# Kernel optimization log

Hardware: AMD Instinct MI355X
Metric: run time of the kernel (lower is better)

## Reference

```python
import jax, jax.numpy as jnp
import numpy as np
import math

B, SEQ, PRED, F, DM, NH, DFF, S, DMARK = 16, 336, 96, 7, 512, 8, 2048, 16, 5
EL, DL = 2, 1
DH = DM // NH


def _pe(max_len, d):
    pos = np.arange(max_len)[:, None].astype(np.float32)
    div = np.exp(np.arange(0, d, 2).astype(np.float32) * (-math.log(10000.0) / d))
    pe = np.zeros((max_len, d), np.float32)
    pe[:, 0::2] = np.sin(pos * div)
    pe[:, 1::2] = np.cos(pos * div)
    return jnp.asarray(pe)


def _make_tao():
    t = np.ones((S, S), np.float32)
    t[:, 0] = 0.0
    t[:, -1] = 0.0
    t[1] *= -1.0
    t[0] = 0.0
    t[0, 0] = 1.0
    t[2:, 1:-1] = np.eye(S - 2, dtype=np.float32)
    return jnp.asarray(t)


PE = _pe(2000, DM)
TAO = _make_tao()
ZVEC = jnp.zeros((S,), jnp.float32).at[:2].set(1.0)
MASK = jnp.triu(jnp.full((PRED, PRED), -1e9, jnp.float32), k=1)  # causal additive mask


def _ln(x, w, b, eps=1e-5):
    m = x.mean(-1, keepdims=True)
    v = ((x - m) ** 2).mean(-1, keepdims=True)
    return (x - m) * jax.lax.rsqrt(v + eps) * w + b


def _mha(q_in, kv_in, qkv_w, qkv_b, ow, ob, mask=None):
    wq, wk, wv = jnp.split(qkv_w, 3, axis=0)
    bq, bk, bv = jnp.split(qkv_b, 3, axis=0)

    def proj(x, w, bb):
        y = x @ w.T + bb  # [B, T, DM]
        return y.reshape(y.shape[0], y.shape[1], NH, DH).transpose(0, 2, 1, 3)

    q, k, v = proj(q_in, wq, bq), proj(kv_in, wk, bk), proj(kv_in, wv, bv)
    s = jnp.einsum('bhqd,bhkd->bhqk', q, k) / math.sqrt(DH)
    if mask is not None:
        s = s + mask
    a = jax.nn.softmax(s, axis=-1)
    o = jnp.einsum('bhqk,bhkd->bhqd', a, v)
    o = o.transpose(0, 2, 1, 3).reshape(q_in.shape)
    return o @ ow.T + ob


def _per_feature(xe, xd, eqw, eqb, eow, eob, el1w, el1b, el2w, el2b,
                 ef1w, ef1b, ef2w, ef2b, elw, elb,
                 dsqw, dsqb, dsow, dsob, dcqw, dcqb, dcow, dcob,
                 dl1w, dl1b, dl2w, dl2b, dl3w, dl3b, df1w, df1b, df2w, df2b):
    # post-norm TransformerEncoder (relu FFN), eval mode (no dropout)
    h = xe
    for l in range(EL):
        h = _ln(h + _mha(h, h, eqw[l], eqb[l], eow[l], eob[l]), el1w[l], el1b[l])
        ff = jax.nn.relu(h @ ef1w[l].T + ef1b[l]) @ ef2w[l].T + ef2b[l]
        h = _ln(h + ff, el2w[l], el2b[l])
    # encoder_linear maps time axis seqlen -> prelen
    mem = jnp.einsum('bsd,ps->bpd', h, elw) + elb[None, :, None]
    t = xd
    for l in range(DL):
        t = _ln(t + _mha(t, t, dsqw[l], dsqb[l], dsow[l], dsob[l], MASK), dl1w[l], dl1b[l])
        t = _ln(t + _mha(t, mem, dcqw[l], dcqb[l], dcow[l], dcob[l]), dl2w[l], dl2b[l])
        ff = jax.nn.relu(t @ df1w[l].T + df1b[l]) @ df2w[l].T + df2b[l]
        t = _ln(t + ff, dl3w[l], dl3b[l])
    return t


_vfeat = jax.vmap(_per_feature, in_axes=(1, 1) + (0,) * 32, out_axes=1)


def setup_inputs():
    key = jax.random.key(0)
    ks = iter(jax.random.split(key, 64))

    def rn(shape, s=0.05):
        return jax.random.normal(next(ks), shape, jnp.float32) * s

    return {
        'batch_x': rn((B, SEQ, F), 1.0),
        'batch_x_mark': rn((B, SEQ, DMARK - 1), 1.0),
        'batch_y': rn((B, PRED, F), 1.0),
        'batch_y_mark': rn((B, PRED, DMARK - 1), 1.0),
        'w_in': rn((DM, DMARK)), 'b_in': rn((DM,)),
        'w_co': rn((DM, DMARK - 1)), 'b_co': rn((DM,)),
        'eqw': rn((F, EL, 3 * DM, DM)), 'eqb': rn((F, EL, 3 * DM)),
        'eow': rn((F, EL, DM, DM)), 'eob': rn((F, EL, DM)),
        'el1w': jnp.ones((F, EL, DM)), 'el1b': jnp.zeros((F, EL, DM)),
        'el2w': jnp.ones((F, EL, DM)), 'el2b': jnp.zeros((F, EL, DM)),
        'ef1w': rn((F, EL, DFF, DM)), 'ef1b': rn((F, EL, DFF)),
        'ef2w': rn((F, EL, DM, DFF)), 'ef2b': rn((F, EL, DM)),
        'elw': rn((F, PRED, SEQ)), 'elb': rn((F, PRED)),
        'dsqw': rn((F, DL, 3 * DM, DM)), 'dsqb': rn((F, DL, 3 * DM)),
        'dsow': rn((F, DL, DM, DM)), 'dsob': rn((F, DL, DM)),
        'dcqw': rn((F, DL, 3 * DM, DM)), 'dcqb': rn((F, DL, 3 * DM)),
        'dcow': rn((F, DL, DM, DM)), 'dcob': rn((F, DL, DM)),
        'dl1w': jnp.ones((F, DL, DM)), 'dl1b': jnp.zeros((F, DL, DM)),
        'dl2w': jnp.ones((F, DL, DM)), 'dl2b': jnp.zeros((F, DL, DM)),
        'dl3w': jnp.ones((F, DL, DM)), 'dl3b': jnp.zeros((F, DL, DM)),
        'df1w': rn((F, DL, DFF, DM)), 'df1b': rn((F, DL, DFF)),
        'df2w': rn((F, DL, DM, DFF)), 'df2b': rn((F, DL, DM)),
        'wc': rn((S, DM)), 'bc': rn((S,)),
        'ws': rn((1, DM)), 'bs': rn((1,)),
    }


def reference(batch_x, batch_x_mark, batch_y, batch_y_mark,
              w_in, b_in, w_co, b_co,
              eqw, eqb, eow, eob, el1w, el1b, el2w, el2b,
              ef1w, ef1b, ef2w, ef2b, elw, elb,
              dsqw, dsqb, dsow, dsob, dcqw, dcqb, dcow, dcob,
              dl1w, dl1b, dl2w, dl2b, dl3w, dl3b, df1w, df1b, df2w, df2b,
              wc, bc, ws, bs):
    Bsz = batch_x.shape[0]
    # time marks are shared across features -> broadcast instead of concat loop
    hist = jnp.concatenate(
        [batch_x[..., None],
         jnp.broadcast_to(batch_x_mark[:, :, None, :], (Bsz, SEQ, F, DMARK - 1))], axis=-1)
    fut = jnp.broadcast_to(batch_y_mark[:, -PRED:, None, :], (Bsz, PRED, F, DMARK - 1))
    hist = hist.transpose(0, 2, 1, 3)  # [B, F, SEQ, DMARK]
    fut = fut.transpose(0, 2, 1, 3)    # [B, F, PRED, DMARK-1]
    xe = hist @ w_in.T + b_in + PE[:SEQ]
    xd = fut @ w_co.T + b_co + PE[:PRED]
    dec = _vfeat(xe, xd, eqw, eqb, eow, eob, el1w, el1b, el2w, el2b,
                 ef1w, ef1b, ef2w, ef2b, elw, elb,
                 dsqw, dsqb, dsow, dsob, dcqw, dcqb, dcow, dcob,
                 dl1w, dl1b, dl2w, dl2b, dl3w, dl3b, df1w, df1b, df2w, df2b)
    # g_c = Linear + Hardsigmoid; g_s = Linear + Softplus
    c = jnp.clip((jnp.einsum('bfpd,sd->bfps', dec, wc) + bc) / 6.0 + 0.5, 0.0, 1.0)
    sig = jax.nn.softplus(jnp.einsum('bfpd,d->bfp', dec, ws[0]) + bs[0])
    # linear state recurrence a = TAO @ a + c, y = z^T a, scanned over prediction days
    a0 = c[:, :, 0]                      # [B, F, S] (torch initializes a with day-0 g_c)
    cs = jnp.moveaxis(c, 2, 0)           # [PRED, B, F, S]
    ss = jnp.moveaxis(sig, 2, 0)         # [PRED, B, F]

    def step(a, xs):
        cd, sd = xs
        a = jnp.einsum('ij,bfj->bfi', TAO, a) + cd
        return a, jnp.einsum('s,bfs->bf', ZVEC, a) + sd

    _, ys = jax.lax.scan(step, a0, (cs, ss))
    return jnp.transpose(ys, (1, 0, 2))  # [B, PRED, F]
```

## Files before the change

kernel.cpp:

```cpp
#include <hip/hip_runtime.h>

typedef unsigned short u16;
typedef unsigned int   u32;
typedef __attribute__((ext_vector_type(8))) short short8;
typedef __attribute__((ext_vector_type(4))) float f32x4;

#define DEV static __device__ __forceinline__

DEV float bf2f(u16 u) { return __uint_as_float(((u32)u) << 16); }
DEV u16 f2bf(float f) {
  u32 u = __float_as_uint(f);
  return (u16)((u + 0x7fffu + ((u >> 16) & 1u)) >> 16);
}

#define GLD16(gp, lp) __builtin_amdgcn_global_load_lds( \
    (__attribute__((address_space(1))) u32*)(gp),       \
    (__attribute__((address_space(3))) u32*)(lp), 16, 0, 0)

__global__ __launch_bounds__(256) void gemm_bf16(
    const u16* __restrict__ A, const u16* __restrict__ Bw, u16* __restrict__ C,
    const float* __restrict__ bias, int M, int N, int K,
    long sAz, long sBz, long sCz, long sBiasZ, int relu)
{
  __shared__ __align__(16) u16 Asm[128 * 32];
  __shared__ __align__(16) u16 Bsm[128 * 32];
  int z = blockIdx.z;
  A += (size_t)z * sAz; Bw += (size_t)z * sBz; C += (size_t)z * sCz; bias += (size_t)z * sBiasZ;
  int tileM = blockIdx.x * 128, tileN = blockIdx.y * 128;
  int tid = threadIdx.x, wave = tid >> 6, lane = tid & 63;

  const u16* gA = A + (size_t)(tileM + wave * 16 + (lane >> 2)) * K + (lane & 3) * 8;
  const u16* gB = Bw + (size_t)(tileN + wave * 16 + (lane >> 2)) * K + (lane & 3) * 8;
  u16* lA = Asm + wave * 512 + lane * 8;
  u16* lB = Bsm + wave * 512 + lane * 8;

  f32x4 acc[4][4] = {};

  int wm = (wave & 1) * 64, wn = (wave >> 1) * 64;
  int lr = lane & 15, lk = (lane >> 4) * 8;
  const u16* ra = Asm + (wm + lr) * 32 + lk;
  const u16* rb = Bsm + (wn + lr) * 32 + lk;

  for (int kt = 0; kt < K; kt += 32) {
    GLD16(gA, lA); GLD16(gA + (size_t)64 * K, lA + 2048);
    GLD16(gB, lB); GLD16(gB + (size_t)64 * K, lB + 2048);
    gA += 32; gB += 32;
    __syncthreads();
    short8 av[4], bv[4];
    #pragma unroll
    for (int i = 0; i < 4; i++) av[i] = *(const short8*)(ra + i * 512);
    #pragma unroll
    for (int j = 0; j < 4; j++) bv[j] = *(const short8*)(rb + j * 512);
    #pragma unroll
    for (int i = 0; i < 4; i++)
      #pragma unroll
      for (int j = 0; j < 4; j++)
        acc[i][j] = __builtin_amdgcn_mfma_f32_16x16x32_bf16(av[i], bv[j], acc[i][j], 0, 0, 0);
    __syncthreads();
  }

  #pragma unroll
  for (int j = 0; j < 4; j++) {
    int ncol = tileN + wn + j * 16 + lr;
    float bb = bias[ncol];
    #pragma unroll
    for (int i = 0; i < 4; i++) {
      int mrow = tileM + wm + i * 16 + (lane >> 4) * 4;
      #pragma unroll
      for (int r = 0; r < 4; r++) {
        float v = acc[i][j][r] + bb;
        if (relu) v = fmaxf(v, 0.f);
        C[(size_t)(mrow + r) * N + ncol] = f2bf(v);
      }
    }
  }
}

__global__ void cvt_w_kernel(const float* __restrict__ src, u16* __restrict__ dst,
                             long n_per_f, long f_stride, long total4)
{
  long i = (long)blockIdx.x * blockDim.x + threadIdx.x;
  long step = (long)gridDim.x * blockDim.x;
  for (; i < total4; i += step) {
    long e = i * 4;
    long f = e / n_per_f; long r = e - f * n_per_f;
    float4 v = *(const float4*)(src + f * f_stride + r);
    *(ushort4*)(dst + e) = make_ushort4(f2bf(v.x), f2bf(v.y), f2bf(v.z), f2bf(v.w));
  }
}

__global__ __launch_bounds__(128) void embed_enc_k(
    const float* __restrict__ x, const float* __restrict__ mark,
    const float* __restrict__ w_in, const float* __restrict__ b_in,
    u16* __restrict__ hb)
{
  int row = blockIdx.x;
  int f = row / 5376; int rem = row - f * 5376; int b = rem / 336; int s = rem - b * 336;
  int bsix = b * 336 + s;
  float v0 = x[(size_t)bsix * 7 + f];
  float m0 = mark[(size_t)bsix * 4 + 0], m1 = mark[(size_t)bsix * 4 + 1];
  float m2 = mark[(size_t)bsix * 4 + 2], m3 = mark[(size_t)bsix * 4 + 3];
  int d0 = threadIdx.x * 4;
  u16 ob[4];
  #pragma unroll
  for (int c = 0; c < 4; c++) {
    int d = d0 + c;
    const float* w = w_in + d * 5;
    float val = w[0] * v0 + w[1] * m0 + w[2] * m1 + w[3] * m2 + w[4] * m3 + b_in[d];
    int i = d >> 1;
    float dv = expf((float)i * -0.0359778920778f);
    float arg = (float)s * dv;
    val += (d & 1) ? cosf(arg) : sinf(arg);
    ob[c] = f2bf(val);
  }
  *(ushort4*)(hb + (size_t)row * 512 + d0) = make_ushort4(ob[0], ob[1], ob[2], ob[3]);
}

__global__ __launch_bounds__(128) void embed_dec_k(
    const float* __restrict__ ymark, const float* __restrict__ w_co,
    const float* __restrict__ b_co, u16* __restrict__ tb)
{
  int row = blockIdx.x;
  int f = row / 1536; int rem = row - f * 1536; int b = rem / 96; int pp = rem - b * 96;
  int bp = b * 96 + pp;
  float m0 = ymark[(size_t)bp * 4 + 0], m1 = ymark[(size_t)bp * 4 + 1];
  float m2 = ymark[(size_t)bp * 4 + 2], m3 = ymark[(size_t)bp * 4 + 3];
  int d0 = threadIdx.x * 4;
  u16 ob[4];
  #pragma unroll
  for (int c = 0; c < 4; c++) {
    int d = d0 + c;
    const float* w = w_co + d * 4;
    float val = w[0] * m0 + w[1] * m1 + w[2] * m2 + w[3] * m3 + b_co[d];
    int i = d >> 1;
    float dv = expf((float)i * -0.0359778920778f);
    float arg = (float)pp * dv;
    val += (d & 1) ? cosf(arg) : sinf(arg);
    ob[c] = f2bf(val);
  }
  *(ushort4*)(tb + (size_t)row * 512 + d0) = make_ushort4(ob[0], ob[1], ob[2], ob[3]);
}

template<int LK>
__global__ __launch_bounds__(256) void attn_mfma(
    const u16* __restrict__ q, const u16* __restrict__ k, const u16* __restrict__ v,
    u16* __restrict__ out, int Lq, int qstride, int kvstride, int causal)
{
  constexpr int NKT = LK / 16;
  constexpr int NKS = (LK + 31) / 32;
  constexpr int KPAD = NKS * 32;
  constexpr int VSTR = 360;

  __shared__ __align__(16) u16 KsS[LK * 64];
  __shared__ __align__(16) u16 VtS[64 * VSTR];
  __shared__ __align__(16) u16 PWS[4][16 * VSTR];

  int hh = blockIdx.x, fb = blockIdx.y;
  int tid = threadIdx.x, wave = tid >> 6, lane = tid & 63;

  const u16* qp = q + (size_t)fb * Lq * qstride + hh * 64;
  const u16* kp = k + (size_t)fb * LK * kvstride + hh * 64;
  const u16* vp = v + (size_t)fb * LK * kvstride + hh * 64;

  {
    int r = (lane >> 3), s = lane & 7;
    for (int r0 = wave * 8; r0 < LK; r0 += 32) {
      int row = r0 + r;
      const u16* src = kp + (size_t)row * kvstride + ((s ^ (row & 7)) * 8);
      GLD16(src, KsS + r0 * 64 + lane * 8);
    }
  }
  for (int idx = tid; idx < LK * 8; idx += 256) {
    int kk = idx >> 3, dg = idx & 7;
    uint4 pv = *(const uint4*)(vp + (size_t)kk * kvstride + dg * 8);
    u16 e0 = (u16)pv.x, e1 = (u16)(pv.x >> 16);
    u16 e2 = (u16)pv.y, e3 = (u16)(pv.y >> 16);
    u16 e4 = (u16)pv.z, e5 = (u16)(pv.z >> 16);
    u16 e6 = (u16)pv.w, e7 = (u16)(pv.w >> 16);
    u16* col = VtS + (size_t)(dg * 8) * VSTR + kk;
    col[0 * VSTR] = e0; col[1 * VSTR] = e1; col[2 * VSTR] = e2; col[3 * VSTR] = e3;
    col[4 * VSTR] = e4; col[5 * VSTR] = e5; col[6 * VSTR] = e6; col[7 * VSTR] = e7;
  }
  if constexpr (KPAD > LK) {
    constexpr int TW = KPAD - LK;
    for (int i = tid; i < 64 * TW; i += 256)
      VtS[(i / TW) * VSTR + LK + (i % TW)] = 0;
    u16* PW = PWS[wave];
    for (int i = lane; i < 16 * TW; i += 64)
      PW[(i / TW) * VSTR + LK + (i % TW)] = 0;
  }
  __syncthreads();

  u16* PW = PWS[wave];
  int lr = lane & 15, lg = lane >> 4;
  int nqt = Lq / 16;

  for (int qt = wave; qt < nqt; qt += 4) {
    const u16* qrow = qp + (size_t)(qt * 16 + lr) * qstride + lg * 8;
    short8 qf0 = *(const short8*)(qrow);
    short8 qf1 = *(const short8*)(qrow + 32);

    f32x4 sacc[NKT];
    #pragma unroll
    for (int t = 0; t < NKT; t++) {
      int row = t * 16 + lr;
      const u16* kb = KsS + row * 64;
      short8 kf0 = *(const short8*)(kb + ((lg) ^ (row & 7)) * 8);
      short8 kf1 = *(const short8*)(kb + ((lg + 4) ^ (row & 7)) * 8);
      f32x4 s = {0.f, 0.f, 0.f, 0.f};
      s = __builtin_amdgcn_mfma_f32_16x16x32_bf16(qf0, kf0, s, 0, 0, 0);
      s = __builtin_amdgcn_mfma_f32_16x16x32_bf16(qf1, kf1, s, 0, 0, 0);
      sacc[t] = s;
    }

    float mx0 = -3e38f, mx1 = -3e38f, mx2 = -3e38f, mx3 = -3e38f;
    #pragma unroll
    for (int t = 0; t < NKT; t++) {
      int kg = t * 16 + lr;
      #pragma unroll
      for (int r = 0; r < 4; r++) {
        float val = sacc[t][r] * 0.125f;
        int qg = qt * 16 + lg * 4 + r;
        if (causal && kg > qg) val = -1e30f;
        sacc[t][r] = val;
        if (r == 0) mx0 = fmaxf(mx0, val);
        if (r == 1) mx1 = fmaxf(mx1, val);
        if (r == 2) mx2 = fmaxf(mx2, val);
        if (r == 3) mx3 = fmaxf(mx3, val);
      }
    }
    #pragma unroll
    for (int m = 1; m < 16; m <<= 1) {
      mx0 = fmaxf(mx0, __shfl_xor(mx0, m));
      mx1 = fmaxf(mx1, __shfl_xor(mx1, m));
      mx2 = fmaxf(mx2, __shfl_xor(mx2, m));
      mx3 = fmaxf(mx3, __shfl_xor(mx3, m));
    }
    float sm0 = 0.f, sm1 = 0.f, sm2 = 0.f, sm3 = 0.f;
    #pragma unroll
    for (int t = 0; t < NKT; t++) {
      float p0 = __expf(sacc[t][0] - mx0);
      float p1 = __expf(sacc[t][1] - mx1);
      float p2 = __expf(sacc[t][2] - mx2);
      float p3 = __expf(sacc[t][3] - mx3);
      sacc[t][0] = p0; sacc[t][1] = p1; sacc[t][2] = p2; sacc[t][3] = p3;
      sm0 += p0; sm1 += p1; sm2 += p2; sm3 += p3;
    }
    #pragma unroll
    for (int m = 1; m < 16; m <<= 1) {
      sm0 += __shfl_xor(sm0, m);
      sm1 += __shfl_xor(sm1, m);
      sm2 += __shfl_xor(sm2, m);
      sm3 += __shfl_xor(sm3, m);
    }
    float inv0 = 1.f / sm0, inv1 = 1.f / sm1, inv2 = 1.f / sm2, inv3 = 1.f / sm3;

    #pragma unroll
    for (int t = 0; t < NKT; t++) {
      u16* pw = PW + (size_t)(lg * 4) * VSTR + t * 16 + lr;
      pw[0 * VSTR] = f2bf(sacc[t][0]);
      pw[1 * VSTR] = f2bf(sacc[t][1]);
      pw[2 * VSTR] = f2bf(sacc[t][2]);
      pw[3 * VSTR] = f2bf(sacc[t][3]);
    }

    f32x4 oacc[4] = {};
    #pragma unroll
    for (int s = 0; s < NKS; s++) {
      short8 pf = *(const short8*)(PW + (size_t)lr * VSTR + s * 32 + lg * 8);
      #pragma unroll
      for (int j = 0; j < 4; j++) {
        short8 vf = *(const short8*)(VtS + (size_t)(j * 16 + lr) * VSTR + s * 32 + lg * 8);
        oacc[j] = __builtin_amdgcn_mfma_f32_16x16x32_bf16(pf, vf, oacc[j], 0, 0, 0);
      }
    }

    #pragma unroll
    for (int r = 0; r < 4; r++) {
      float inv = (r == 0) ? inv0 : (r == 1) ? inv1 : (r == 2) ? inv2 : inv3;
      size_t orow = (size_t)fb * Lq + qt * 16 + lg * 4 + r;
      u16* ob = out + orow * 512 + hh * 64 + lr;
      #pragma unroll
      for (int j = 0; j < 4; j++)
        ob[j * 16] = f2bf(oacc[j][r] * inv);
    }
  }
}

__global__ __launch_bounds__(128) void ln_kernel(
    u16* __restrict__ h, const u16* __restrict__ delta,
    const float* __restrict__ gamma, const float* __restrict__ beta,
    int rows_per_f, long gstride)
{
  __shared__ float red[2];
  int row = blockIdx.x;
  int f = row / rows_per_f;
  const float* g = gamma + (size_t)f * gstride;
  const float* be = beta + (size_t)f * gstride;
  int d0 = threadIdx.x * 4;
  size_t p = (size_t)row * 512 + d0;
  ushort4 hv = *(const ushort4*)(h + p);
  ushort4 dv = *(const ushort4*)(delta + p);
  float x0 = bf2f(hv.x) + bf2f(dv.x), x1 = bf2f(hv.y) + bf2f(dv.y);
  float x2 = bf2f(hv.z) + bf2f(dv.z), x3 = bf2f(hv.w) + bf2f(dv.w);
  float ssum = x0 + x1 + x2 + x3;
  #pragma unroll
  for (int m = 1; m < 64; m <<= 1) ssum += __shfl_xor(ssum, m);
  if ((threadIdx.x & 63) == 0) red[threadIdx.x >> 6] = ssum;
  __syncthreads();
  float mean = (red[0] + red[1]) * (1.f / 512.f);
  __syncthreads();
  float c0 = x0 - mean, c1 = x1 - mean, c2 = x2 - mean, c3 = x3 - mean;
  float sq = c0 * c0 + c1 * c1 + c2 * c2 + c3 * c3;
  #pragma unroll
  for (int m = 1; m < 64; m <<= 1) sq += __shfl_xor(sq, m);
  if ((threadIdx.x & 63) == 0) red[threadIdx.x >> 6] = sq;
  __syncthreads();
  float var = (red[0] + red[1]) * (1.f / 512.f);
  float rstd = rsqrtf(var + 1e-5f);
  float y0 = c0 * rstd * g[d0 + 0] + be[d0 + 0];
  float y1 = c1 * rstd * g[d0 + 1] + be[d0 + 1];
  float y2 = c2 * rstd * g[d0 + 2] + be[d0 + 2];
  float y3 = c3 * rstd * g[d0 + 3] + be[d0 + 3];
  *(ushort4*)(h + p) = make_ushort4(f2bf(y0), f2bf(y1), f2bf(y2), f2bf(y3));
}

__global__ __launch_bounds__(256) void mem_kernel(
    const u16* __restrict__ h, const float* __restrict__ elw,
    const float* __restrict__ elb, u16* __restrict__ memb)
{
  int fb = blockIdx.x; int f = fb >> 4;
  int pc = blockIdx.y;
  int d0 = threadIdx.x * 2;
  const u16* hbase = h + (size_t)fb * 336 * 512;
  const float* wbase = elw + (size_t)f * 96 * 336 + (size_t)pc * 16 * 336;
  float a0[16], a1[16];
  #pragma unroll
  for (int pp = 0; pp < 16; pp++) { a0[pp] = 0.f; a1[pp] = 0.f; }
  for (int s = 0; s < 336; s++) {
    ushort2 h2 = *(const ushort2*)(hbase + (size_t)s * 512 + d0);
    float hx = bf2f(h2.x), hy = bf2f(h2.y);
    #pragma unroll
    for (int pp = 0; pp < 16; pp++) {
      float w = wbase[pp * 336 + s];
      a0[pp] += w * hx; a1[pp] += w * hy;
    }
  }
  #pragma unroll
  for (int pp = 0; pp < 16; pp++) {
    int pidx = pc * 16 + pp;
    size_t row = (size_t)fb * 96 + pidx;
    float e = elb[f * 96 + pidx];
    *(ushort2*)(memb + row * 512 + d0) = make_ushort2(f2bf(a0[pp] + e), f2bf(a1[pp] + e));
  }
}

__global__ __launch_bounds__(64) void head_kernel(
    const u16* __restrict__ td, const float* __restrict__ wcp, const float* __restrict__ bcp,
    const float* __restrict__ wsp, const float* __restrict__ bsp,
    float* __restrict__ cb, float* __restrict__ sg, int f0)
{
  int rl = blockIdx.x, lane = threadIdx.x;
  size_t row = (size_t)f0 * 1536 + rl;
  const u16* x = td + (size_t)rl * 512;
  float xr[8];
  #pragma unroll
  for (int j = 0; j < 8; j++) xr[j] = bf2f(x[lane + 64 * j]);
  #pragma unroll
  for (int o = 0; o < 16; o++) {
    const float* w = wcp + o * 512;
    float p = 0.f;
    #pragma unroll
    for (int j = 0; j < 8; j++) p += xr[j] * w[lane + 64 * j];
    #pragma unroll
    for (int m = 1; m < 64; m <<= 1) p += __shfl_xor(p, m);
    if (lane == 0) {
      float cv = (p + bcp[o]) / 6.0f + 0.5f;
      cb[row * 16 + o] = fminf(fmaxf(cv, 0.f), 1.f);
    }
  }
  float p = 0.f;
  #pragma unroll
  for (int j = 0; j < 8; j++) p += xr[j] * wsp[lane + 64 * j];
  #pragma unroll
  for (int m = 1; m < 64; m <<= 1) p += __shfl_xor(p, m);
  if (lane == 0) {
    float zv = p + bsp[0];
    sg[row] = (zv > 20.f) ? zv : log1pf(expf(zv));
  }
}

__global__ __launch_bounds__(256) void scan_kernel(
    const float* __restrict__ cbuf, const float* __restrict__ sgb, float* __restrict__ outp)
{
  int f = blockIdx.x;
  int b = threadIdx.x >> 4;
  int s = threadIdx.x & 15;
  size_t rbase = ((size_t)f * 16 + b) * 96;
  float a = cbuf[rbase * 16 + s];
  for (int p = 0; p < 96; ++p) {
    float cd = cbuf[(rbase + p) * 16 + s];
    float sd = sgb[rbase + p];
    float xs = (s >= 1 && s <= 14) ? a : 0.f;
    #pragma unroll
    for (int m = 1; m < 16; m <<= 1) xs += __shfl_xor(xs, m);
    float up = __shfl_up(a, 1, 16);
    float an = (s == 0) ? (a + cd) : ((s == 1) ? (cd - xs) : (up + cd));
    a = an;
    float y01 = __shfl(a, 0, 16) + __shfl(a, 1, 16) + sd;
    if (s == 0) outp[((size_t)b * 96 + p) * 7 + f] = y01;
  }
}

__global__ void diag_kernel(float* __restrict__ out, float v, int n)
{
  int i = blockIdx.x * 256 + threadIdx.x;
  if (i < n) out[i] = v;
}

extern "C" void kernel_launch(void* const* d_in, const int* in_sizes, int n_in,
                              void* d_out, int out_size, void* d_ws, size_t ws_size,
                              hipStream_t stream)
{
  (void)in_sizes; (void)n_in;
  const float* batch_x      = (const float*)d_in[0];
  const float* batch_x_mark = (const float*)d_in[1];
  const float* batch_y_mark = (const float*)d_in[3];
  const float* w_in = (const float*)d_in[4];
  const float* b_in = (const float*)d_in[5];
  const float* w_co = (const float*)d_in[6];
  const float* b_co = (const float*)d_in[7];
  const float* eqw  = (const float*)d_in[8];
  const float* eqb  = (const float*)d_in[9];
  const float* eow  = (const float*)d_in[10];
  const float* eob  = (const float*)d_in[11];
  const float* el1w = (const float*)d_in[12];
  const float* el1b = (const float*)d_in[13];
  const float* el2w = (const float*)d_in[14];
  const float* el2b = (const float*)d_in[15];
  const float* ef1w = (const float*)d_in[16];
  const float* ef1b = (const float*)d_in[17];
  const float* ef2w = (const float*)d_in[18];
  const float* ef2b = (const float*)d_in[19];
  const float* elw  = (const float*)d_in[20];
  const float* elb  = (const float*)d_in[21];
  const float* dsqw = (const float*)d_in[22];
  const float* dsqb = (const float*)d_in[23];
  const float* dsow = (const float*)d_in[24];
  const float* dsob = (const float*)d_in[25];
  const float* dcqw = (const float*)d_in[26];
  const float* dcqb = (const float*)d_in[27];
  const float* dcow = (const float*)d_in[28];
  const float* dcob = (const float*)d_in[29];
  const float* dl1w = (const float*)d_in[30];
  const float* dl1b = (const float*)d_in[31];
  const float* dl2w = (const float*)d_in[32];
  const float* dl2b = (const float*)d_in[33];
  const float* dl3w = (const float*)d_in[34];
  const float* dl3b = (const float*)d_in[35];
  const float* df1w = (const float*)d_in[36];
  const float* df1b = (const float*)d_in[37];
  const float* df2w = (const float*)d_in[38];
  const float* df2b = (const float*)d_in[39];
  const float* wc   = (const float*)d_in[40];
  const float* bc   = (const float*)d_in[41];
  const float* wsg  = (const float*)d_in[42];
  const float* bsg  = (const float*)d_in[43];

  const size_t NE = 37632;
  const size_t ND = 10752;
  auto al = [](size_t x) { return (x + 255) & ~(size_t)255; };

  size_t fixedB = al(NE * 1024) + al(ND * 1024) + al(ND * 64) + al(ND * 4);
  int G = 0;
  for (int g = 7; g >= 1; --g) {
    size_t need = fixedB
        + al((size_t)g * 5376 * 2048 * 2)
        + al((size_t)g * 5376 * 512 * 2)
        + al((size_t)g * 2048 * 512 * 2)
        + al((size_t)g * 1536 * 512 * 2);
    if (need <= ws_size) { G = g; break; }
  }
  if (G == 0) {
    diag_kernel<<<dim3((out_size + 255) / 256), 256, 0, stream>>>(
        (float*)d_out, 1000.0f + (float)(ws_size >> 20), out_size);
    return;
  }

  char* base = (char*)d_ws;
  size_t off = 0;
  auto alloc = [&](size_t bytes) -> void* { void* r = base + off; off += al(bytes); return r; };
  u16*   hres = (u16*)  alloc(NE * 1024);
  u16*   tres = (u16*)  alloc(ND * 1024);
  float* cb   = (float*)alloc(ND * 64);
  float* sg   = (float*)alloc(ND * 4);
  u16*   bigc = (u16*)  alloc((size_t)G * 5376 * 2048 * 2);
  u16*   aobc = (u16*)  alloc((size_t)G * 5376 * 512 * 2);
  u16*   wbuf = (u16*)  alloc((size_t)G * 2048 * 512 * 2);
  u16*   memb = (u16*)  alloc((size_t)G * 1536 * 512 * 2);

  embed_enc_k<<<dim3(37632), 128, 0, stream>>>(batch_x, batch_x_mark, w_in, b_in, hres);
  embed_dec_k<<<dim3(10752), 128, 0, stream>>>(batch_y_mark, w_co, b_co, tres);

  auto cvtw = [&](const float* src, long n_per_f, long f_stride, int g) {
    cvt_w_kernel<<<dim3(512), 256, 0, stream>>>(src, wbuf, n_per_f, f_stride,
                                                (long)g * n_per_f / 4);
  };
  auto gemm = [&](const u16* A, long sAz, u16* C, long sCz, const float* bias, long sBias,
                  int M, int N, int K, int g, int relu) {
    dim3 gr(M / 128, N / 128, g);
    gemm_bf16<<<gr, 256, 0, stream>>>(A, wbuf, C, bias, M, N, K, sAz, (long)N * K, sCz,
                                      sBias, relu);
  };

  for (int f0 = 0; f0 < 7; f0 += G) {
    int g = (7 - f0 < G) ? (7 - f0) : G;
    u16* hc = hres + (size_t)f0 * 5376 * 512;
    u16* tc = tres + (size_t)f0 * 1536 * 512;

    for (int l = 0; l < 2; ++l) {
      cvtw(eqw + (size_t)f0 * 1572864 + (size_t)l * 786432, 786432L, 1572864L, g);
      gemm(hc, 5376L * 512, bigc, 5376L * 1536, eqb + f0 * 3072 + l * 1536, 3072,
           5376, 1536, 512, g, 0);
      attn_mfma<336><<<dim3(8, g * 16), 256, 0, stream>>>(
          bigc, bigc + 512, bigc + 1024, aobc, 336, 1536, 1536, 0);
      cvtw(eow + (size_t)f0 * 524288 + (size_t)l * 262144, 262144L, 524288L, g);
      gemm(aobc, 5376L * 512, bigc, 5376L * 512, eob + f0 * 1024 + l * 512, 1024,
           5376, 512, 512, g, 0);
      ln_kernel<<<dim3(g * 5376), 128, 0, stream>>>(
          hc, bigc, el1w + f0 * 1024 + l * 512, el1b + f0 * 1024 + l * 512, 5376, 1024);
      cvtw(ef1w + (size_t)f0 * 2097152 + (size_t)l * 1048576, 1048576L, 2097152L, g);
      gemm(hc, 5376L * 512, bigc, 5376L * 2048, ef1b + f0 * 4096 + l * 2048, 4096,
           5376, 2048, 512, g, 1);
      cvtw(ef2w + (size_t)f0 * 2097152 + (size_t)l * 1048576, 1048576L, 2097152L, g);
      gemm(bigc, 5376L * 2048, aobc, 5376L * 512, ef2b + f0 * 1024 + l * 512, 1024,
           5376, 512, 2048, g, 0);
      ln_kernel<<<dim3(g * 5376), 128, 0, stream>>>(
          hc, aobc, el2w + f0 * 1024 + l * 512, el2b + f0 * 1024 + l * 512, 5376, 1024);
    }

    mem_kernel<<<dim3(g * 16, 6), 256, 0, stream>>>(
        hc, elw + (size_t)f0 * 32256, elb + f0 * 96, memb);

    cvtw(dsqw + (size_t)f0 * 786432, 786432L, 786432L, g);
    gemm(tc, 1536L * 512, bigc, 1536L * 1536, dsqb + f0 * 1536, 1536,
         1536, 1536, 512, g, 0);
    attn_mfma<96><<<dim3(8, g * 16), 256, 0, stream>>>(
        bigc, bigc + 512, bigc + 1024, aobc, 96, 1536, 1536, 1);
    cvtw(dsow + (size_t)f0 * 262144, 262144L, 262144L, g);
    gemm(aobc, 1536L * 512, bigc, 1536L * 512, dsob + f0 * 512, 512,
         1536, 512, 512, g, 0);
    ln_kernel<<<dim3(g * 1536), 128, 0, stream>>>(
        tc, bigc, dl1w + f0 * 512, dl1b + f0 * 512, 1536, 512);

    cvtw(dcqw + (size_t)f0 * 786432, 262144L, 786432L, g);
    gemm(tc, 1536L * 512, bigc, 1536L * 512, dcqb + f0 * 1536, 1536,
         1536, 512, 512, g, 0);
    u16* bigKV = bigc + (size_t)g * 1536 * 512;
    cvtw(dcqw + (size_t)f0 * 786432 + 262144, 524288L, 786432L, g);
    gemm(memb, 1536L * 512, bigKV, 1536L * 1024, dcqb + f0 * 1536 + 512, 1536,
         1536, 1024, 512, g, 0);
    attn_mfma<96><<<dim3(8, g * 16), 256, 0, stream>>>(
        bigc, bigKV, bigKV + 512, aobc, 96, 512, 1024, 0);
    cvtw(dcow + (size_t)f0 * 262144, 262144L, 262144L, g);
    gemm(aobc, 1536L * 512, bigc, 1536L * 512, dcob + f0 * 512, 512,
         1536, 512, 512, g, 0);
    ln_kernel<<<dim3(g * 1536), 128, 0, stream>>>(
        tc, bigc, dl2w + f0 * 512, dl2b + f0 * 512, 1536, 512);

    cvtw(df1w + (size_t)f0 * 1048576, 1048576L, 1048576L, g);
    gemm(tc, 1536L * 512, bigc, 1536L * 2048, df1b + f0 * 2048, 2048,
         1536, 2048, 512, g, 1);
    cvtw(df2w + (size_t)f0 * 1048576, 1048576L, 1048576L, g);
    gemm(bigc, 1536L * 2048, aobc, 1536L * 512, df2b + f0 * 512, 512,
         1536, 512, 2048, g, 0);
    ln_kernel<<<dim3(g * 1536), 128, 0, stream>>>(
        tc, aobc, dl3w + f0 * 512, dl3b + f0 * 512, 1536, 512);

    head_kernel<<<dim3(g * 1536), 64, 0, stream>>>(tc, wc, bc, wsg, bsg, cb, sg, f0);
  }

  scan_kernel<<<dim3(7), 256, 0, stream>>>(cb, sg, (float*)d_out);
}
```

Baseline: 1.757 ms.

## Rewrite bf16 GEMM with 256x256 tiles, double-buffered swizzled LDS and XCD remap

Rewrites the batched bf16 GEMM to use 256x256 output tiles with 512 threads, each wave computing 128x64, and a K step of 64. Tiles are staged into two LDS buffers with an XOR swizzle to avoid bank conflicts. The next tile is prefetched while MFMAs run on the current one, with explicit vmcnt waits and barriers. Block IDs are remapped so neighbouring tiles land on the same XCD, and MFMA sections run at raised wave priority. The larger tiles raise arithmetic intensity but produce far fewer blocks and use much more LDS, which risks underfilling the GPU on the smaller GEMMs.

```diff
diff --git a/kernel.cpp b/kernel.cpp
--- a/kernel.cpp
+++ b/kernel.cpp
@@ -17,60 +17,96 @@
     (__attribute__((address_space(1))) u32*)(gp),       \
     (__attribute__((address_space(3))) u32*)(lp), 16, 0, 0)
 
-__global__ __launch_bounds__(256) void gemm_bf16(
+__global__ __launch_bounds__(512, 2) void gemm_bf16(
     const u16* __restrict__ A, const u16* __restrict__ Bw, u16* __restrict__ C,
     const float* __restrict__ bias, int M, int N, int K,
     long sAz, long sBz, long sCz, long sBiasZ, int relu)
 {
-  __shared__ __align__(16) u16 Asm[128 * 32];
-  __shared__ __align__(16) u16 Bsm[128 * 32];
-  int z = blockIdx.z;
-  A += (size_t)z * sAz; Bw += (size_t)z * sBz; C += (size_t)z * sCz; bias += (size_t)z * sBiasZ;
-  int tileM = blockIdx.x * 128, tileN = blockIdx.y * 128;
+  __shared__ __align__(16) u16 Asm[2][256 * 64];
+  __shared__ __align__(16) u16 Bsm[2][256 * 64];
+
+  int gx = (int)gridDim.x, gy = (int)gridDim.y;
+  int nwg = gx * gy * (int)gridDim.z;
+  int orig = (int)blockIdx.x + gx * ((int)blockIdx.y + gy * (int)blockIdx.z);
+  int q = nwg >> 3, r = nwg & 7;
+  int xcd = orig & 7, pos = orig >> 3;
+  int lg_id = (xcd < r) ? (xcd * (q + 1) + pos) : (r * (q + 1) + (xcd - r) * q + pos);
+  int bz = lg_id / (gx * gy);
+  int rem = lg_id - bz * (gx * gy);
+  int by = rem / gx, bx = rem - by * gx;
+
+  A += (size_t)bz * sAz; Bw += (size_t)bz * sBz; C += (size_t)bz * sCz; bias += (size_t)bz * sBiasZ;
+  int tileM = bx * 256, tileN = by * 256;
   int tid = threadIdx.x, wave = tid >> 6, lane = tid & 63;
-
-  const u16* gA = A + (size_t)(tileM + wave * 16 + (lane >> 2)) * K + (lane & 3) * 8;
-  const u16* gB = Bw + (size_t)(tileN + wave * 16 + (lane >> 2)) * K + (lane & 3) * 8;
-  u16* lA = Asm + wave * 512 + lane * 8;
-  u16* lB = Bsm + wave * 512 + lane * 8;
-
-  f32x4 acc[4][4] = {};
-
-  int wm = (wave & 1) * 64, wn = (wave >> 1) * 64;
-  int lr = lane & 15, lk = (lane >> 4) * 8;
-  const u16* ra = Asm + (wm + lr) * 32 + lk;
-  const u16* rb = Bsm + (wn + lr) * 32 + lk;
-
-  for (int kt = 0; kt < K; kt += 32) {
-    GLD16(gA, lA); GLD16(gA + (size_t)64 * K, lA + 2048);
-    GLD16(gB, lB); GLD16(gB + (size_t)64 * K, lB + 2048);
-    gA += 32; gB += 32;
-    __syncthreads();
-    short8 av[4], bv[4];
-    #pragma unroll
-    for (int i = 0; i < 4; i++) av[i] = *(const short8*)(ra + i * 512);
-    #pragma unroll
-    for (int j = 0; j < 4; j++) bv[j] = *(const short8*)(rb + j * 512);
-    #pragma unroll
-    for (int i = 0; i < 4; i++)
+  int lr = lane & 15, lgp = lane >> 4;
+  int wm = (wave >> 2) * 128;
+  int wn = (wave & 3) * 64;
+
+  const int NT = K >> 6;
+
+  auto STAGE = [&](int b, int t) {
+    int kb = t * 64;
+    #pragma unroll
+    for (int i = 0; i < 4; i++) {
+      int gi = i * 512 + wave * 64 + lane;
+      int row = gi >> 3, g = gi & 7;
+      int gsw = (g ^ (row & 7)) * 8;
+      GLD16(A + (size_t)(tileM + row) * K + kb + gsw, &Asm[b][(size_t)gi * 8]);
+      GLD16(Bw + (size_t)(tileN + row) * K + kb + gsw, &Bsm[b][(size_t)gi * 8]);
+    }
+  };
+
+  f32x4 acc[8][4] = {};
+
+  STAGE(0, 0);
+  if (NT > 1) STAGE(1, 1);
+
+  for (int t = 0; t < NT; ++t) {
+    int cur = t & 1;
+    if (t + 1 < NT) asm volatile("s_waitcnt vmcnt(8)" ::: "memory");
+    else            asm volatile("s_waitcnt vmcnt(0)" ::: "memory");
+    asm volatile("s_barrier" ::: "memory");
+
+    const u16* Ab = Asm[cur];
+    const u16* Bb = Bsm[cur];
+    #pragma unroll
+    for (int ks = 0; ks < 2; ++ks) {
+      short8 bfr[4], afr[8];
       #pragma unroll
-      for (int j = 0; j < 4; j++)
-        acc[i][j] = __builtin_amdgcn_mfma_f32_16x16x32_bf16(av[i], bv[j], acc[i][j], 0, 0, 0);
-    __syncthreads();
-  }
-
-  #pragma unroll
-  for (int j = 0; j < 4; j++) {
-    int ncol = tileN + wn + j * 16 + lr;
+      for (int n = 0; n < 4; ++n) {
+        int row = wn + n * 16 + lr;
+        bfr[n] = *(const short8*)(Bb + row * 64 + (((ks * 4 + lgp) ^ (row & 7)) * 8));
+      }
+      #pragma unroll
+      for (int m = 0; m < 8; ++m) {
+        int row = wm + m * 16 + lr;
+        afr[m] = *(const short8*)(Ab + row * 64 + (((ks * 4 + lgp) ^ (row & 7)) * 8));
+      }
+      __builtin_amdgcn_s_setprio(1);
+      #pragma unroll
+      for (int m = 0; m < 8; ++m)
+        #pragma unroll
+        for (int n = 0; n < 4; ++n)
+          acc[m][n] = __builtin_amdgcn_mfma_f32_16x16x32_bf16(afr[m], bfr[n], acc[m][n], 0, 0, 0);
+      __builtin_amdgcn_s_setprio(0);
+    }
+    asm volatile("s_waitcnt lgkmcnt(0)" ::: "memory");
+    asm volatile("s_barrier" ::: "memory");
+    if (t + 2 < NT) STAGE(cur, t + 2);
+  }
+
+  #pragma unroll
+  for (int n = 0; n < 4; ++n) {
+    int ncol = tileN + wn + n * 16 + lr;
     float bb = bias[ncol];
     #pragma unroll
-    for (int i = 0; i < 4; i++) {
-      int mrow = tileM + wm + i * 16 + (lane >> 4) * 4;
+    for (int m = 0; m < 8; ++m) {
+      int mrow = tileM + wm + m * 16 + lgp * 4;
       #pragma unroll
-      for (int r = 0; r < 4; r++) {
-        float v = acc[i][j][r] + bb;
+      for (int rr = 0; rr < 4; ++rr) {
+        float v = acc[m][n][rr] + bb;
         if (relu) v = fmaxf(v, 0.f);
-        C[(size_t)(mrow + r) * N + ncol] = f2bf(v);
+        C[(size_t)(mrow + rr) * N + ncol] = f2bf(v);
       }
     }
   }
@@ -508,8 +544,8 @@
   };
   auto gemm = [&](const u16* A, long sAz, u16* C, long sCz, const float* bias, long sBias,
                   int M, int N, int K, int g, int relu) {
-    dim3 gr(M / 128, N / 128, g);
-    gemm_bf16<<<gr, 256, 0, stream>>>(A, wbuf, C, bias, M, N, K, sAz, (long)N * K, sCz,
+    dim3 gr(M / 256, N / 256, g);
+    gemm_bf16<<<gr, 512, 0, stream>>>(A, wbuf, C, bias, M, N, K, sAz, (long)N * K, sCz,
                                       sBias, relu);
   };
 
```

Result: no change. 1.766 ms (+0.5%).
